# Optimization experiments

Hardware: AMD Instinct MI355X
Metric: run time of the kernel (lower is better)

## Reference

```python
import jax, jax.numpy as jnp
import numpy as np

EPS = 1e-5  # torch LayerNorm default eps
L2_EPS = 1e-12


def _l2norm(t, axis=-1):
    return t / jnp.sqrt(jnp.sum(t * t, axis=axis, keepdims=True) + L2_EPS)


def setup_inputs() -> dict:
    key = jax.random.key(0)
    k1, k2, k3 = jax.random.split(key, 3)
    b, n, d = 4, 2048, 1024
    h, e, cs = 8, 16, 2048
    x = jax.random.normal(k1, (b, n, d), dtype=jnp.float32)
    # xavier_normal_ on [h, d, e]: fan_in = d*e, fan_out = h*e
    std = float(np.sqrt(2.0 / (d * e + h * e)))
    rand_projs = jax.random.normal(k2, (h, d, e), dtype=jnp.float32) * std
    codebook = jax.random.normal(k3, (h, cs, e), dtype=jnp.float32)
    return {"x": x, "rand_projs": rand_projs, "codebook": codebook}


def reference(x, rand_projs, codebook):
    # LayerNorm over last dim, no affine
    mu = jnp.mean(x, axis=-1, keepdims=True)
    var = jnp.mean((x - mu) ** 2, axis=-1, keepdims=True)
    xn = (x - mu) / jnp.sqrt(var + EPS)
    # per-head random projection: [b,n,d] x [h,d,e] -> [b,n,h,e]
    proj = jnp.einsum('bnd,hde->bnhe', xn, rand_projs)
    # cosine-sim VQ per head: normalize both, argmax similarity
    q = _l2norm(proj, axis=-1)                 # [b,n,h,e]
    cb = _l2norm(codebook, axis=-1)            # [h,c,e]
    sim = jnp.einsum('bnhe,hce->bnhc', q, cb)  # [b,n,h,c]
    indices = jnp.argmax(sim, axis=-1)         # [b,n,h] int
    return indices
```

## Files before the change

### kernel.cpp

```cpp
#include <hip/hip_runtime.h>
#include <math.h>


typedef short bf16x8 __attribute__((ext_vector_type(8)));
typedef float f32x4 __attribute__((ext_vector_type(4)));

__device__ __forceinline__ void stage16(const float* g, float* lds_base) {
  __builtin_amdgcn_global_load_lds(
      (const __attribute__((address_space(1))) void*)g,
      (__attribute__((address_space(3))) void*)lds_base, 16, 0, 0);
}

__device__ __forceinline__ unsigned short f2bf(float f) {
  unsigned u = __builtin_bit_cast(unsigned, f);
  unsigned r = (u + 0x7FFFu + ((u >> 16) & 1u)) >> 16;
  return (unsigned short)r;
}
__device__ __forceinline__ float bf2f(unsigned short b) {
  return __builtin_bit_cast(float, (unsigned)b << 16);
}
__device__ __forceinline__ void split3(float v, unsigned short& h,
                                       unsigned short& m, unsigned short& l) {
  h = f2bf(v);
  float r = v - bf2f(h);
  m = f2bf(r);
  float r2 = r - bf2f(m);
  l = f2bf(r2);
}

__global__ __launch_bounds__(256) void k_cbnorm(const float* __restrict__ cb,
                                                unsigned short* __restrict__ ch,
                                                unsigned short* __restrict__ cm,
                                                unsigned short* __restrict__ cl) {
  int v = blockIdx.x * 256 + threadIdx.x;
  const float4* p = (const float4*)(cb + (size_t)v * 16);
  float4 q0 = p[0], q1 = p[1], q2 = p[2], q3 = p[3];
  float f[16] = {q0.x,q0.y,q0.z,q0.w, q1.x,q1.y,q1.z,q1.w,
                 q2.x,q2.y,q2.z,q2.w, q3.x,q3.y,q3.z,q3.w};
  double s = 0.0;
#pragma unroll
  for (int i = 0; i < 16; ++i) s += (double)f[i] * (double)f[i];
  double inv = 1.0 / sqrt(s + 1e-12);
  unsigned short vh[16], vm[16], vl[16];
#pragma unroll
  for (int i = 0; i < 16; ++i)
    split3((float)((double)f[i] * inv), vh[i], vm[i], vl[i]);
#pragma unroll
  for (int i = 0; i < 2; ++i) {
    ((bf16x8*)(ch + (size_t)v * 16))[i] = ((bf16x8*)vh)[i];
    ((bf16x8*)(cm + (size_t)v * 16))[i] = ((bf16x8*)vm)[i];
    ((bf16x8*)(cl + (size_t)v * 16))[i] = ((bf16x8*)vl)[i];
  }
}

__global__ __launch_bounds__(256) void k_colsum(const float* __restrict__ W,
                                                float* __restrict__ cs) {
  __shared__ float red[16][17];
  int h = blockIdx.x;
  int e = threadIdx.x & 15, part = threadIdx.x >> 4;
  const float* base = W + h * 16384 + e;
  float s = 0.f;
  int d0 = part * 64;
  for (int i = 0; i < 64; ++i) s += base[(d0 + i) * 16];
  red[e][part] = s;
  __syncthreads();
  if (threadIdx.x < 16) {
    float t = 0.f;
#pragma unroll
    for (int p = 0; p < 16; ++p) t += red[threadIdx.x][p];
    cs[h * 16 + threadIdx.x] = t;
  }
}

__global__ __launch_bounds__(256) void k_wsplit(const float* __restrict__ W,
                                                unsigned short* __restrict__ Wth,
                                                unsigned short* __restrict__ Wtm,
                                                unsigned short* __restrict__ Wtl) {
  int idx = blockIdx.x * 256 + threadIdx.x;
  int d = idx & 1023, col = idx >> 10;
  int h = col >> 4, e = col & 15;
  float v = W[h * 16384 + d * 16 + e];
  unsigned short a, b, c;
  split3(v, a, b, c);
  Wth[(size_t)col * 1024 + d] = a;
  Wtm[(size_t)col * 1024 + d] = b;
  Wtl[(size_t)col * 1024 + d] = c;
}

__global__ __launch_bounds__(256) void k_mu(const float* __restrict__ x,
                                            float* __restrict__ mu) {
  __shared__ float red[16][17];
  const int t = threadIdx.x;
  const int g = t & 15, tg = t >> 4;
  const int row = blockIdx.x * 16 + tg;
  const float4* xr = (const float4*)(x + (size_t)row * 1024);
  float s = 0.f;
#pragma unroll
  for (int m = 0; m < 16; ++m) {
    float4 v = xr[g + 16 * m];
    s += (v.x + v.y) + (v.z + v.w);
  }
  red[tg][g] = s;
  __syncthreads();
  if (g == 0) {
    float tt = 0.f;
#pragma unroll
    for (int k = 0; k < 16; ++k) tt += red[tg][k];
    mu[row] = tt * (1.0f / 1024.0f);
  }
}

__global__ __launch_bounds__(256) void k_proj(const float* __restrict__ x,
                                              const unsigned short* __restrict__ Wth,
                                              const unsigned short* __restrict__ Wtm,
                                              const unsigned short* __restrict__ Wtl,
                                              float* __restrict__ part) {
  __shared__ __align__(16) float sXf[4096];
  __shared__ __align__(16) unsigned short sB[12288];
  const int t = threadIdx.x;
  const int lane = t & 63, w = t >> 6;
  const int r0 = blockIdx.x * 128;
  const int ks = blockIdx.y;
  const int q = lane >> 4, n16 = lane & 15;
  const int qe = q & 1;
  const bool qlt2 = (q < 2);
  const int a1off = qlt2 ? 0 : 4096;
  const int a2off = qlt2 ? 4096 : 0;
  const int a3off = qlt2 ? 8192 : 0;

  f32x4 acc[2][8];
#pragma unroll
  for (int rt = 0; rt < 2; ++rt)
#pragma unroll
    for (int h = 0; h < 8; ++h) acc[rt][h] = (f32x4){0.f, 0.f, 0.f, 0.f};

  for (int win = 0; win < 4; ++win) {
    const int dbase = ks * 128 + win * 32;
    __syncthreads();
#pragma unroll
    for (int i = 0; i < 4; ++i) {
      int c = i * 256 + t;
      int u = c >> 1, half = c & 1;
      int oct = u >> 7, row = u & 127;
      stage16(x + (size_t)(r0 + row) * 1024 + dbase + oct * 8 + half * 4,
              sXf + (i * 256 + w * 64) * 4);
    }
#pragma unroll
    for (int i = 0; i < 6; ++i) {
      int c = i * 256 + t;
      int a = c >> 9, rem = c & 511;
      int oct = rem >> 7, col = rem & 127;
      const unsigned short* Wa = (a == 0) ? Wth : ((a == 1) ? Wtm : Wtl);
      stage16((const float*)(Wa + (size_t)col * 1024 + dbase + oct * 8),
              (float*)sB + (i * 256 + w * 64) * 4);
    }
    __syncthreads();

#pragma unroll
    for (int dc2 = 0; dc2 < 2; ++dc2) {
      const int oct = dc2 * 2 + qe;
      bf16x8 av1[2], av3[2];
#pragma unroll
      for (int rt = 0; rt < 2; ++rt) {
        const int row = w * 32 + rt * 16 + n16;
        const float* xp = sXf + (oct * 128 + row) * 8;
        float4 xa = *(const float4*)(xp);
        float4 xb = *(const float4*)(xp + 4);
        float xf[8] = {xa.x, xa.y, xa.z, xa.w, xb.x, xb.y, xb.z, xb.w};
        unsigned short s1[8], s3[8];
#pragma unroll
        for (int j = 0; j < 8; ++j) {
          unsigned short hh, mm, ll;
          split3(xf[j], hh, mm, ll);
          s1[j] = qlt2 ? hh : mm;
          s3[j] = qlt2 ? hh : ll;
        }
        av1[rt] = *(bf16x8*)s1;
        av3[rt] = *(bf16x8*)s3;
      }
#pragma unroll
      for (int h = 0; h < 8; ++h) {
        const int u = oct * 128 + h * 16 + n16;
        bf16x8 b1 = *(const bf16x8*)(sB + (a1off + u * 8));
        bf16x8 b2 = *(const bf16x8*)(sB + (a2off + u * 8));
        bf16x8 b3 = *(const bf16x8*)(sB + (a3off + u * 8));
#pragma unroll
        for (int rt = 0; rt < 2; ++rt) {
          acc[rt][h] = __builtin_amdgcn_mfma_f32_16x16x32_bf16(av1[rt], b1, acc[rt][h], 0, 0, 0);
          acc[rt][h] = __builtin_amdgcn_mfma_f32_16x16x32_bf16(av1[rt], b2, acc[rt][h], 0, 0, 0);
          acc[rt][h] = __builtin_amdgcn_mfma_f32_16x16x32_bf16(av3[rt], b3, acc[rt][h], 0, 0, 0);
        }
      }
    }
  }

  float* po = part + ((size_t)ks * 8192 + r0) * 128;
#pragma unroll
  for (int rt = 0; rt < 2; ++rt)
#pragma unroll
    for (int h = 0; h < 8; ++h)
#pragma unroll
      for (int r = 0; r < 4; ++r)
        po[(size_t)(w * 32 + rt * 16 + q * 4 + r) * 128 + h * 16 + n16] =
            acc[rt][h][r];
}

__global__ __launch_bounds__(256) void k_combine(const float* __restrict__ part,
                                                 const float* __restrict__ mu,
                                                 const float* __restrict__ csum,
                                                 unsigned short* __restrict__ ph,
                                                 unsigned short* __restrict__ pm,
                                                 unsigned short* __restrict__ pl) {
  int idx = blockIdx.x * 256 + threadIdx.x;
  int row = idx >> 5, c4 = (idx & 31) * 4;
  float4 a = {0.f, 0.f, 0.f, 0.f};
#pragma unroll
  for (int s = 0; s < 8; ++s) {
    float4 p = *(const float4*)(part + ((size_t)s * 8192 + row) * 128 + c4);
    a.x += p.x; a.y += p.y; a.z += p.z; a.w += p.w;
  }
  float4 cs = *(const float4*)(csum + c4);
  float m = mu[row];
  float o[4] = {a.x - m * cs.x, a.y - m * cs.y, a.z - m * cs.z, a.w - m * cs.w};
  unsigned short vh[4], vm[4], vl[4];
#pragma unroll
  for (int k = 0; k < 4; ++k) split3(o[k], vh[k], vm[k], vl[k]);
  int head = c4 >> 4, e0 = c4 & 15;
  size_t base = ((size_t)head * 8192 + row) * 16 + e0;
  *(short4*)(ph + base) = *(short4*)vh;
  *(short4*)(pm + base) = *(short4*)vm;
  *(short4*)(pl + base) = *(short4*)vl;
}

__global__ __launch_bounds__(256) void k_argmax(
    const unsigned short* __restrict__ ph, const unsigned short* __restrict__ pm,
    const unsigned short* __restrict__ pl, const unsigned short* __restrict__ ch,
    const unsigned short* __restrict__ cm, const unsigned short* __restrict__ cl,
    float* __restrict__ amv, int* __restrict__ ami) {
  const int t = threadIdx.x;
  const int lane = t & 63, w = t >> 6;
  const int h = blockIdx.y;
  const int z = blockIdx.z;
  const int r0 = blockIdx.x * 256 + w * 64;
  const int q = lane >> 4;
  const int n16 = lane & 15;
  const int ehalf = (q & 1) * 8;
  const bool qlt2 = (q < 2);

  const unsigned short* pa1 = qlt2 ? ph : pm;
  const unsigned short* pa3 = qlt2 ? ph : pl;
  bf16x8 a1[4], a3[4];
#pragma unroll
  for (int rt = 0; rt < 4; ++rt) {
    size_t off = ((size_t)h * 8192 + r0 + rt * 16 + n16) * 16 + ehalf;
    a1[rt] = *(const bf16x8*)(pa1 + off);
    a3[rt] = *(const bf16x8*)(pa3 + off);
  }

  float best[4][4];
  int   bidx[4][4];
#pragma unroll
  for (int rt = 0; rt < 4; ++rt)
#pragma unroll
    for (int r = 0; r < 4; ++r) { best[rt][r] = -3.402823466e38f; bidx[rt][r] = 0; }

  const unsigned short* pb1 = qlt2 ? ch : cm;
  const unsigned short* pb2 = qlt2 ? cm : ch;
  const unsigned short* pb3 = qlt2 ? cl : ch;
  const size_t cbase = ((size_t)h * 2048 + z * 512) * 16;

  for (int tile = 0; tile < 32; ++tile) {
    size_t off = cbase + (size_t)(tile * 16 + n16) * 16 + ehalf;
    bf16x8 b1 = *(const bf16x8*)(pb1 + off);
    bf16x8 b2 = *(const bf16x8*)(pb2 + off);
    bf16x8 b3 = *(const bf16x8*)(pb3 + off);
    const int code = z * 512 + tile * 16 + n16;
#pragma unroll
    for (int rt = 0; rt < 4; ++rt) {
      f32x4 acc = {0.f, 0.f, 0.f, 0.f};
      acc = __builtin_amdgcn_mfma_f32_16x16x32_bf16(a1[rt], b1, acc, 0, 0, 0);
      acc = __builtin_amdgcn_mfma_f32_16x16x32_bf16(a1[rt], b2, acc, 0, 0, 0);
      acc = __builtin_amdgcn_mfma_f32_16x16x32_bf16(a3[rt], b3, acc, 0, 0, 0);
#pragma unroll
      for (int r = 0; r < 4; ++r)
        if (acc[r] > best[rt][r]) { best[rt][r] = acc[r]; bidx[rt][r] = code; }
    }
  }

#pragma unroll
  for (int off = 8; off >= 1; off >>= 1) {
#pragma unroll
    for (int rt = 0; rt < 4; ++rt)
#pragma unroll
      for (int r = 0; r < 4; ++r) {
        float ov = __shfl_xor(best[rt][r], off, 16);
        int   oi = __shfl_xor(bidx[rt][r], off, 16);
        if (ov > best[rt][r] || (ov == best[rt][r] && oi < bidx[rt][r])) {
          best[rt][r] = ov; bidx[rt][r] = oi;
        }
      }
  }
  if (n16 == 0) {
#pragma unroll
    for (int rt = 0; rt < 4; ++rt)
#pragma unroll
      for (int r = 0; r < 4; ++r) {
        int row = r0 + rt * 16 + q * 4 + r;
        size_t o = (size_t)z * 65536 + (size_t)row * 8 + h;
        amv[o] = best[rt][r]; ami[o] = bidx[rt][r];
      }
  }
}

__global__ __launch_bounds__(256) void k_amred(const float* __restrict__ amv,
                                               const int* __restrict__ ami,
                                               int* __restrict__ out) {
  int i = blockIdx.x * 256 + threadIdx.x;
  float bv = amv[i]; int bi = ami[i];
#pragma unroll
  for (int z = 1; z < 4; ++z) {
    float v = amv[(size_t)z * 65536 + i];
    if (v > bv) { bv = v; bi = ami[(size_t)z * 65536 + i]; }
  }
  out[i] = bi;
}

extern "C" void kernel_launch(void* const* d_in, const int* in_sizes, int n_in,
                              void* d_out, int out_size, void* d_ws, size_t ws_size,
                              hipStream_t stream) {
  (void)in_sizes; (void)n_in; (void)out_size; (void)ws_size;
  const float* x  = (const float*)d_in[0];
  const float* rp = (const float*)d_in[1];
  const float* cb = (const float*)d_in[2];
  int* out = (int*)d_out;

  float* ws = (float*)d_ws;
  float*          csum = ws;
  float*          mu   = ws + 128;
  float*          part = ws + 8320;
  unsigned short* Wth  = (unsigned short*)(ws + 8396928);
  unsigned short* Wtm  = (unsigned short*)(ws + 8462464);
  unsigned short* Wtl  = (unsigned short*)(ws + 8528000);
  unsigned short* ch   = (unsigned short*)(ws + 8593536);
  unsigned short* cm   = (unsigned short*)(ws + 8724608);
  unsigned short* cl   = (unsigned short*)(ws + 8855680);
  unsigned short* ph   = (unsigned short*)(ws + 8986752);
  unsigned short* pm   = (unsigned short*)(ws + 9511040);
  unsigned short* pl   = (unsigned short*)(ws + 10035328);
  float*          amv  = ws + 10559616;
  int*            ami  = (int*)(ws + 10821760);

  hipLaunchKernelGGL(k_cbnorm,  dim3(64),        dim3(256), 0, stream, cb, ch, cm, cl);
  hipLaunchKernelGGL(k_colsum,  dim3(8),         dim3(256), 0, stream, rp, csum);
  hipLaunchKernelGGL(k_wsplit,  dim3(512),       dim3(256), 0, stream, rp, Wth, Wtm, Wtl);
  hipLaunchKernelGGL(k_mu,      dim3(512),       dim3(256), 0, stream, x, mu);
  hipLaunchKernelGGL(k_proj,    dim3(64, 8),     dim3(256), 0, stream, x, Wth, Wtm, Wtl, part);
  hipLaunchKernelGGL(k_combine, dim3(1024),      dim3(256), 0, stream, part, mu, csum, ph, pm, pl);
  hipLaunchKernelGGL(k_argmax,  dim3(32, 8, 4),  dim3(256), 0, stream, ph, pm, pl, ch, cm, cl, amv, ami);
  hipLaunchKernelGGL(k_amred,   dim3(256),       dim3(256), 0, stream, amv, ami, out);
}
```

Before: 156.7 us.

## Drop LDS staging in projection, double the grids, prefetch codebook tiles

The projection kernel now loads x and the split weights straight from global memory into registers instead of staging them in LDS with barriers. Each block covers 64 rows instead of 128, so the grid doubles. The argmax kernel splits the codebook into 8 slices instead of 4 and software-prefetches the next codebook tile into registers. The final reduction is widened to match and the argmax index buffer is moved. The aim is to raise occupancy and parallelism and remove barrier stalls. In exchange, x is re-split more often and global and L2 traffic for weight reads goes up.

```diff
diff --git a/kernel.cpp b/kernel.cpp
--- a/kernel.cpp
+++ b/kernel.cpp
@@ -4,12 +4,6 @@
 
 typedef short bf16x8 __attribute__((ext_vector_type(8)));
 typedef float f32x4 __attribute__((ext_vector_type(4)));
-
-__device__ __forceinline__ void stage16(const float* g, float* lds_base) {
-  __builtin_amdgcn_global_load_lds(
-      (const __attribute__((address_space(1))) void*)g,
-      (__attribute__((address_space(3))) void*)lds_base, 16, 0, 0);
-}
 
 __device__ __forceinline__ unsigned short f2bf(float f) {
   unsigned u = __builtin_bit_cast(unsigned, f);
@@ -115,94 +109,55 @@
                                               const unsigned short* __restrict__ Wtm,
                                               const unsigned short* __restrict__ Wtl,
                                               float* __restrict__ part) {
-  __shared__ __align__(16) float sXf[4096];
-  __shared__ __align__(16) unsigned short sB[12288];
   const int t = threadIdx.x;
   const int lane = t & 63, w = t >> 6;
-  const int r0 = blockIdx.x * 128;
+  const int r0 = blockIdx.x * 64;
   const int ks = blockIdx.y;
   const int q = lane >> 4, n16 = lane & 15;
-  const int qe = q & 1;
   const bool qlt2 = (q < 2);
-  const int a1off = qlt2 ? 0 : 4096;
-  const int a2off = qlt2 ? 4096 : 0;
-  const int a3off = qlt2 ? 8192 : 0;
-
-  f32x4 acc[2][8];
-#pragma unroll
-  for (int rt = 0; rt < 2; ++rt)
-#pragma unroll
-    for (int h = 0; h < 8; ++h) acc[rt][h] = (f32x4){0.f, 0.f, 0.f, 0.f};
-
-  for (int win = 0; win < 4; ++win) {
-    const int dbase = ks * 128 + win * 32;
-    __syncthreads();
-#pragma unroll
-    for (int i = 0; i < 4; ++i) {
-      int c = i * 256 + t;
-      int u = c >> 1, half = c & 1;
-      int oct = u >> 7, row = u & 127;
-      stage16(x + (size_t)(r0 + row) * 1024 + dbase + oct * 8 + half * 4,
-              sXf + (i * 256 + w * 64) * 4);
+  const int row = r0 + w * 16 + n16;
+
+  const unsigned short* pb1 = qlt2 ? Wth : Wtm;
+  const unsigned short* pb2 = qlt2 ? Wtm : Wth;
+  const unsigned short* pb3 = qlt2 ? Wtl : Wth;
+
+  f32x4 acc[8];
+#pragma unroll
+  for (int h = 0; h < 8; ++h) acc[h] = (f32x4){0.f, 0.f, 0.f, 0.f};
+
+  for (int dg = 0; dg < 8; ++dg) {
+    const int dq = ks * 128 + dg * 16 + (q & 1) * 8;
+    float4 xa = *(const float4*)(x + (size_t)row * 1024 + dq);
+    float4 xb = *(const float4*)(x + (size_t)row * 1024 + dq + 4);
+    float xf[8] = {xa.x, xa.y, xa.z, xa.w, xb.x, xb.y, xb.z, xb.w};
+    unsigned short s1[8], s3[8];
+#pragma unroll
+    for (int j = 0; j < 8; ++j) {
+      unsigned short hh, mm, ll;
+      split3(xf[j], hh, mm, ll);
+      s1[j] = qlt2 ? hh : mm;
+      s3[j] = qlt2 ? hh : ll;
     }
-#pragma unroll
-    for (int i = 0; i < 6; ++i) {
-      int c = i * 256 + t;
-      int a = c >> 9, rem = c & 511;
-      int oct = rem >> 7, col = rem & 127;
-      const unsigned short* Wa = (a == 0) ? Wth : ((a == 1) ? Wtm : Wtl);
-      stage16((const float*)(Wa + (size_t)col * 1024 + dbase + oct * 8),
-              (float*)sB + (i * 256 + w * 64) * 4);
+    bf16x8 a1 = *(bf16x8*)s1;
+    bf16x8 a3 = *(bf16x8*)s3;
+#pragma unroll
+    for (int h = 0; h < 8; ++h) {
+      size_t wo = (size_t)(h * 16 + n16) * 1024 + dq;
+      bf16x8 b1 = *(const bf16x8*)(pb1 + wo);
+      bf16x8 b2 = *(const bf16x8*)(pb2 + wo);
+      bf16x8 b3 = *(const bf16x8*)(pb3 + wo);
+      acc[h] = __builtin_amdgcn_mfma_f32_16x16x32_bf16(a1, b1, acc[h], 0, 0, 0);
+      acc[h] = __builtin_amdgcn_mfma_f32_16x16x32_bf16(a1, b2, acc[h], 0, 0, 0);
+      acc[h] = __builtin_amdgcn_mfma_f32_16x16x32_bf16(a3, b3, acc[h], 0, 0, 0);
     }
-    __syncthreads();
-
-#pragma unroll
-    for (int dc2 = 0; dc2 < 2; ++dc2) {
-      const int oct = dc2 * 2 + qe;
-      bf16x8 av1[2], av3[2];
-#pragma unroll
-      for (int rt = 0; rt < 2; ++rt) {
-        const int row = w * 32 + rt * 16 + n16;
-        const float* xp = sXf + (oct * 128 + row) * 8;
-        float4 xa = *(const float4*)(xp);
-        float4 xb = *(const float4*)(xp + 4);
-        float xf[8] = {xa.x, xa.y, xa.z, xa.w, xb.x, xb.y, xb.z, xb.w};
-        unsigned short s1[8], s3[8];
-#pragma unroll
-        for (int j = 0; j < 8; ++j) {
-          unsigned short hh, mm, ll;
-          split3(xf[j], hh, mm, ll);
-          s1[j] = qlt2 ? hh : mm;
-          s3[j] = qlt2 ? hh : ll;
-        }
-        av1[rt] = *(bf16x8*)s1;
-        av3[rt] = *(bf16x8*)s3;
-      }
-#pragma unroll
-      for (int h = 0; h < 8; ++h) {
-        const int u = oct * 128 + h * 16 + n16;
-        bf16x8 b1 = *(const bf16x8*)(sB + (a1off + u * 8));
-        bf16x8 b2 = *(const bf16x8*)(sB + (a2off + u * 8));
-        bf16x8 b3 = *(const bf16x8*)(sB + (a3off + u * 8));
-#pragma unroll
-        for (int rt = 0; rt < 2; ++rt) {
-          acc[rt][h] = __builtin_amdgcn_mfma_f32_16x16x32_bf16(av1[rt], b1, acc[rt][h], 0, 0, 0);
-          acc[rt][h] = __builtin_amdgcn_mfma_f32_16x16x32_bf16(av1[rt], b2, acc[rt][h], 0, 0, 0);
-          acc[rt][h] = __builtin_amdgcn_mfma_f32_16x16x32_bf16(av3[rt], b3, acc[rt][h], 0, 0, 0);
-        }
-      }
-    }
-  }
-
-  float* po = part + ((size_t)ks * 8192 + r0) * 128;
-#pragma unroll
-  for (int rt = 0; rt < 2; ++rt)
-#pragma unroll
-    for (int h = 0; h < 8; ++h)
-#pragma unroll
-      for (int r = 0; r < 4; ++r)
-        po[(size_t)(w * 32 + rt * 16 + q * 4 + r) * 128 + h * 16 + n16] =
-            acc[rt][h][r];
+  }
+
+  float* po = part + ((size_t)ks * 8192 + r0 + w * 16) * 128;
+#pragma unroll
+  for (int h = 0; h < 8; ++h)
+#pragma unroll
+    for (int r = 0; r < 4; ++r)
+      po[(size_t)(q * 4 + r) * 128 + h * 16 + n16] = acc[h][r];
 }
 
 __global__ __launch_bounds__(256) void k_combine(const float* __restrict__ part,
@@ -267,14 +222,22 @@
   const unsigned short* pb1 = qlt2 ? ch : cm;
   const unsigned short* pb2 = qlt2 ? cm : ch;
   const unsigned short* pb3 = qlt2 ? cl : ch;
-  const size_t cbase = ((size_t)h * 2048 + z * 512) * 16;
-
-  for (int tile = 0; tile < 32; ++tile) {
-    size_t off = cbase + (size_t)(tile * 16 + n16) * 16 + ehalf;
-    bf16x8 b1 = *(const bf16x8*)(pb1 + off);
-    bf16x8 b2 = *(const bf16x8*)(pb2 + off);
-    bf16x8 b3 = *(const bf16x8*)(pb3 + off);
-    const int code = z * 512 + tile * 16 + n16;
+  const size_t cbase = ((size_t)h * 2048 + z * 256) * 16;
+
+  size_t off0 = cbase + (size_t)n16 * 16 + ehalf;
+  bf16x8 b1 = *(const bf16x8*)(pb1 + off0);
+  bf16x8 b2 = *(const bf16x8*)(pb2 + off0);
+  bf16x8 b3 = *(const bf16x8*)(pb3 + off0);
+
+  for (int tile = 0; tile < 16; ++tile) {
+    bf16x8 nb1, nb2, nb3;
+    if (tile < 15) {
+      size_t noff = cbase + (size_t)((tile + 1) * 16 + n16) * 16 + ehalf;
+      nb1 = *(const bf16x8*)(pb1 + noff);
+      nb2 = *(const bf16x8*)(pb2 + noff);
+      nb3 = *(const bf16x8*)(pb3 + noff);
+    }
+    const int code = z * 256 + tile * 16 + n16;
 #pragma unroll
     for (int rt = 0; rt < 4; ++rt) {
       f32x4 acc = {0.f, 0.f, 0.f, 0.f};
@@ -285,6 +248,7 @@
       for (int r = 0; r < 4; ++r)
         if (acc[r] > best[rt][r]) { best[rt][r] = acc[r]; bidx[rt][r] = code; }
     }
+    b1 = nb1; b2 = nb2; b3 = nb3;
   }
 
 #pragma unroll
@@ -318,7 +282,7 @@
   int i = blockIdx.x * 256 + threadIdx.x;
   float bv = amv[i]; int bi = ami[i];
 #pragma unroll
-  for (int z = 1; z < 4; ++z) {
+  for (int z = 1; z < 8; ++z) {
     float v = amv[(size_t)z * 65536 + i];
     if (v > bv) { bv = v; bi = ami[(size_t)z * 65536 + i]; }
   }
@@ -348,14 +312,14 @@
   unsigned short* pm   = (unsigned short*)(ws + 9511040);
   unsigned short* pl   = (unsigned short*)(ws + 10035328);
   float*          amv  = ws + 10559616;
-  int*            ami  = (int*)(ws + 10821760);
+  int*            ami  = (int*)(ws + 11083904);
 
   hipLaunchKernelGGL(k_cbnorm,  dim3(64),        dim3(256), 0, stream, cb, ch, cm, cl);
   hipLaunchKernelGGL(k_colsum,  dim3(8),         dim3(256), 0, stream, rp, csum);
   hipLaunchKernelGGL(k_wsplit,  dim3(512),       dim3(256), 0, stream, rp, Wth, Wtm, Wtl);
   hipLaunchKernelGGL(k_mu,      dim3(512),       dim3(256), 0, stream, x, mu);
-  hipLaunchKernelGGL(k_proj,    dim3(64, 8),     dim3(256), 0, stream, x, Wth, Wtm, Wtl, part);
+  hipLaunchKernelGGL(k_proj,    dim3(128, 8),    dim3(256), 0, stream, x, Wth, Wtm, Wtl, part);
   hipLaunchKernelGGL(k_combine, dim3(1024),      dim3(256), 0, stream, part, mu, csum, ph, pm, pl);
-  hipLaunchKernelGGL(k_argmax,  dim3(32, 8, 4),  dim3(256), 0, stream, ph, pm, pl, ch, cm, cl, amv, ami);
+  hipLaunchKernelGGL(k_argmax,  dim3(32, 8, 8),  dim3(256), 0, stream, ph, pm, pl, ch, cm, cl, amv, ami);
   hipLaunchKernelGGL(k_amred,   dim3(256),       dim3(256), 0, stream, amv, ami, out);
 }
```

Result: slower. 224.3 us (+43.2%).
